# Kernel optimization log

Hardware: AMD Instinct MI355X
Metric: run time of the kernel (lower is better)

Reference implementation:

```python
import jax, jax.numpy as jnp
import numpy as np

B, N, H, D, F = 32, 128, 256, 256, 512   # batch, nodes, gru hidden, latent dim, mlp hidden
SUP = 0.5                                 # ancestor_suppression_strength
EPS = 1e-6


def _gru(x, h, Wx, Wh, bx, bh):
    """torch.nn.GRUCell math; x,h: [..., H]."""
    gx = x @ Wx + bx
    gh = h @ Wh + bh
    rx, ux, nx = jnp.split(gx, 3, axis=-1)
    rh, uh, nh = jnp.split(gh, 3, axis=-1)
    r = jax.nn.sigmoid(rx + rh)
    u = jax.nn.sigmoid(ux + uh)
    n = jnp.tanh(nx + r * nh)
    return (1.0 - u) * n + u * h


def setup_inputs() -> dict:
    key = jax.random.key(0)
    ks = jax.random.split(key, 12)
    rn = lambda k, shape, fan: jax.random.normal(k, shape, jnp.float32) * (fan ** -0.5)
    return {
        "z": jax.random.normal(ks[0], (B, D), jnp.float32),
        "targets": jax.random.randint(ks[1], (B, N, N), 0, 2, jnp.int32),
        "W_init": rn(ks[2], (D, H), D),
        "b_init": jnp.zeros((H,), jnp.float32),
        "Wx": rn(ks[3], (H, 3 * H), H),
        "Wh": rn(ks[4], (H, 3 * H), H),
        "bx": jnp.zeros((3 * H,), jnp.float32),
        "bh": jnp.zeros((3 * H,), jnp.float32),
        "W1": rn(ks[5], (2 * H + D, F), 2 * H + D),
        "b1": jnp.zeros((F,), jnp.float32),
        "W2": rn(ks[6], (F, 1), F),
        "b2": jnp.zeros((1,), jnp.float32),
    }


def reference(z, targets, W_init, b_init, Wx, Wh, bx, bh, W1, b1, W2, b2):
    # teacher-forcing link targets: strictly lower-triangular (parents have smaller index)
    tgt = jnp.tril(targets.astype(jnp.float32), k=-1)  # [B,N,N]
    idx = jnp.arange(N)

    def decode_one(z1, t1):  # z1:[D], t1:[N,N]
        h0 = jnp.tanh(z1 @ W_init + b_init)                      # decoder_init: z -> node-0 state
        states0 = jnp.zeros((N, H), jnp.float32).at[0].set(h0)
        A0 = jnp.zeros((N, N), jnp.float32)                      # ancestor bitset: A[i,j]=1 iff j ancestor of i

        def step(carry, t):
            states, A, ll = carry
            m = (idx < t).astype(jnp.float32)                    # existing-node mask
            pooled = (states * m[:, None]).sum(0) / m.sum()      # mean aggregation
            h_prov = _gru(pooled, h0, Wx, Wh, bx, bh)            # provisional new-node state
            # parent logits: MLP([h_new, h_j, z]) for every existing node j
            feat = jnp.concatenate([jnp.broadcast_to(h_prov, (N, H)), states,
                                    jnp.broadcast_to(z1, (N, D))], axis=-1)   # [N, 2H+D]
            logits = (jax.nn.relu(feat @ W1 + b1) @ W2 + b2)[:, 0]            # [N]
            row = t1[t]                                          # teacher-forced parents of node t
            anc = jnp.minimum(row @ A, 1.0)                      # j already ancestor of a chosen parent
            q = jnp.clip(jax.nn.sigmoid(logits) * (1.0 - SUP * anc), EPS, 1.0 - EPS)
            ll = ll + (m * (row * jnp.log(q) + (1.0 - row) * jnp.log1p(-q))).sum()
            A = A.at[t].set(jnp.minimum(row + row @ A, 1.0))     # ancestors(t) = parents U their ancestors
            states = states.at[t].set(h_prov)
            m2 = (idx <= t).astype(jnp.float32)[:, None]
            pooled2 = (states * m2).sum(0) / m2.sum()
            upd = _gru(jnp.broadcast_to(pooled2, (N, H)), states, Wx, Wh, bx, bh)
            states = m2 * upd + (1.0 - m2) * states              # propagate info among generated nodes
            return (states, A, ll), None

        (states, A, ll), _ = jax.lax.scan(step, (states0, A0, jnp.zeros((), jnp.float32)),
                                          jnp.arange(1, N))
        return t1, ll                                            # link matrix (teacher forced), log-likelihood

    L, ll = jax.vmap(decode_one)(z, tgt)
    return L, ll
```

## Files before the change

### kernel.cpp

```cpp
#include <hip/hip_runtime.h>
#include <hip/hip_bf16.h>
#include <math.h>

#define Bz 32
#define Nn 128
#define Hh 256
#define Dd 256
#define Ff 512
#define Gg 768
#define NT 512

typedef short v8s __attribute__((ext_vector_type(8)));
typedef float f4  __attribute__((ext_vector_type(4)));
#define MFMA(a,b,c) __builtin_amdgcn_mfma_f32_16x16x32_bf16(a,b,c,0,0,0)

#define WS_H0    0
#define WS_GH0   (WS_H0 + Bz*Hh)
#define WS_ZW1   (WS_GH0 + Bz*Gg)
#define WS_XH    (WS_ZW1 + Bz*Ff)
#define WS_PSX   (WS_XH + Bz*Hh)
#define WS_LOGP  (WS_PSX + Bz*Hh)
#define WS_BAR   (WS_LOGP + Bz*8*Nn)
#define WS_XS    (WS_BAR + Bz*32)
#define WS_WB    (WS_XS + Bz*16384)
#define WS_TOTAL (WS_WB + 160*2048)

#define SM_SW    0
#define SM_SST   81920
#define SM_NLDS  147456
#define SM_PS    155648
#define SM_HPF   156672
#define SM_GX1   157696
#define SM_GX2   158080
#define SM_BASE  158464
#define SM_BXS   158720
#define SM_BHS   159104
#define SM_GH0S  159488
#define SM_ZB1S  159872
#define SM_H0S   160128
#define SM_PSN   160256
#define SM_LOGI  160384
#define SM_ROWT  160896
#define SM_AMASK 161408
#define SM_ANCW  163456
#define SMEM_SZ  163488

__device__ __forceinline__ unsigned short f2bf(float x) {
  unsigned u = __float_as_uint(x);
  u = u + 0x7fffu + ((u >> 16) & 1u);
  return (unsigned short)(u >> 16);
}
__device__ __forceinline__ unsigned pack2(float e, float o) {
  return (unsigned)f2bf(e) | ((unsigned)f2bf(o) << 16);
}
__device__ __forceinline__ unsigned pkbf(float x, float y) {
  __hip_bfloat162 h = __float22bfloat162_rn(make_float2(x, y));
  union { __hip_bfloat162 h; unsigned u; } c; c.h = h; return c.u;
}
__device__ __forceinline__ float bf2f(unsigned short s) {
  return __uint_as_float(((unsigned)s) << 16);
}
__device__ __forceinline__ float sigm(float x) { return 1.0f / (1.0f + __expf(-x)); }
__device__ __forceinline__ float tanh_fast(float x) { return 2.0f / (1.0f + __expf(-2.0f*x)) - 1.0f; }
__device__ __forceinline__ v8s u4v(uint4 q) { union { uint4 q; v8s v; } c; c.q = q; return c.v; }

__device__ __forceinline__ void ast32(unsigned* p, unsigned v) {
  __hip_atomic_store(p, v, __ATOMIC_RELAXED, __HIP_MEMORY_SCOPE_AGENT);
}
__device__ __forceinline__ unsigned ald32(const unsigned* p) {
  return __hip_atomic_load(p, __ATOMIC_RELAXED, __HIP_MEMORY_SCOPE_AGENT);
}
__device__ __forceinline__ void ast64(unsigned long long* p, unsigned long long v) {
  __hip_atomic_store(p, v, __ATOMIC_RELAXED, __HIP_MEMORY_SCOPE_AGENT);
}
__device__ __forceinline__ unsigned long long ald64(const unsigned long long* p) {
  return __hip_atomic_load(p, __ATOMIC_RELAXED, __HIP_MEMORY_SCOPE_AGENT);
}

__device__ __forceinline__ void bbar(unsigned* cnt, unsigned& seq)
{
  __builtin_amdgcn_s_waitcnt(0x0F70);
  __syncthreads();
  seq += 8;
  if (threadIdx.x == 0) {
    __hip_atomic_fetch_add(cnt, 1u, __ATOMIC_RELAXED, __HIP_MEMORY_SCOPE_AGENT);
    while (__hip_atomic_load(cnt, __ATOMIC_RELAXED, __HIP_MEMORY_SCOPE_AGENT) < seq)
      __builtin_amdgcn_s_sleep(1);
  }
  __syncthreads();
}

__global__ void __launch_bounds__(256) prep_init(
    const int* __restrict__ tg, const float* __restrict__ Wx,
    const float* __restrict__ Wh, const float* __restrict__ W1,
    float* __restrict__ ws, float* __restrict__ out)
{
  const int stride = gridDim.x * blockDim.x;
  const int t0 = blockIdx.x * blockDim.x + threadIdx.x;

  for (int i = t0; i < Bz*Nn*Nn; i += stride) {
    int col = i & (Nn-1), row = (i >> 7) & (Nn-1);
    out[i] = (col < row) ? (float)tg[i] : 0.0f;
  }
  for (int i = t0; i < Bz; i += stride) out[Bz*Nn*Nn + i] = 0.0f;

  unsigned* BARu = (unsigned*)(ws + WS_BAR);
  for (int i = t0; i < Bz*32; i += stride) BARu[i] = 0u;

  unsigned* Wb = (unsigned*)(ws + WS_WB);
  for (int i = t0; i < 160*2048; i += stride) {
    int jw = i & 3, l = (i >> 2) & 63, ks = (i >> 8) & 7, nt = i >> 11;
    int k = ks*32 + (l >> 4)*8 + 2*jw;
    int n16 = l & 15;
    float lo, hi;
    if (nt < 48)       { int c = nt*16 + n16;        lo = Wh[k*Gg + c];      hi = Wh[(k+1)*Gg + c]; }
    else if (nt < 80)  { int f = (nt-48)*16 + n16;   lo = W1[(Hh+k)*Ff + f]; hi = W1[(Hh+k+1)*Ff + f]; }
    else if (nt < 128) { int c = (nt-80)*16 + n16;   lo = Wx[k*Gg + c];      hi = Wx[(k+1)*Gg + c]; }
    else               { int f = (nt-128)*16 + n16;  lo = W1[k*Ff + f];      hi = W1[(k+1)*Ff + f]; }
    Wb[i] = pack2(lo, hi);
  }
}

__global__ void __launch_bounds__(256) prep_batch(
    const float* __restrict__ z, const float* __restrict__ Wi,
    const float* __restrict__ bi, const float* __restrict__ Wh,
    const float* __restrict__ bh, const float* __restrict__ W1,
    float* __restrict__ ws)
{
  const int b = blockIdx.x, tid = threadIdx.x;
  __shared__ float zs[Dd], h0s[Hh];
  zs[tid] = z[b*Dd + tid];
  __syncthreads();
  float acc = bi[tid];
  for (int d = 0; d < Dd; ++d) acc = fmaf(zs[d], Wi[d*Hh + tid], acc);
  const float h0 = tanhf(acc);
  h0s[tid] = h0;
  ws[WS_H0 + b*Hh + tid] = h0;
  __syncthreads();
  for (int g = tid; g < Gg; g += 256) {
    float a = bh[g];
    for (int h = 0; h < Hh; ++h) a = fmaf(h0s[h], Wh[h*Gg + g], a);
    ws[WS_GH0 + b*Gg + g] = a;
  }
  for (int f = tid; f < Ff; f += 256) {
    float a = 0.0f;
    for (int d = 0; d < Dd; ++d) a = fmaf(zs[d], W1[(2*Hh + d)*Ff + f], a);
    ws[WS_ZW1 + b*Ff + f] = a;
  }
}

__device__ __forceinline__ void build_mv(const float* __restrict__ vec, int quad, v8s* av)
{
  #pragma unroll
  for (int ks = 0; ks < 8; ++ks) {
    const float4 a = *(const float4*)(vec + ks*32 + quad*8);
    const float4 c = *(const float4*)(vec + ks*32 + quad*8 + 4);
    union { unsigned u[4]; v8s v; } cv;
    cv.u[0] = pkbf(a.x, a.y); cv.u[1] = pkbf(a.z, a.w);
    cv.u[2] = pkbf(c.x, c.y); cv.u[3] = pkbf(c.z, c.w);
    av[ks] = cv.v;
  }
}
__device__ __forceinline__ void build_mv2(const float* __restrict__ va,
                                          const float* __restrict__ vb, int quad, v8s* av)
{
  #pragma unroll
  for (int ks = 0; ks < 8; ++ks) {
    const float4 a = *(const float4*)(va + ks*32 + quad*8);
    const float4 b = *(const float4*)(vb + ks*32 + quad*8);
    const float4 c = *(const float4*)(va + ks*32 + quad*8 + 4);
    const float4 d = *(const float4*)(vb + ks*32 + quad*8 + 4);
    union { unsigned u[4]; v8s v; } cv;
    cv.u[0] = pkbf(a.x+b.x, a.y+b.y); cv.u[1] = pkbf(a.z+b.z, a.w+b.w);
    cv.u[2] = pkbf(c.x+d.x, c.y+d.y); cv.u[3] = pkbf(c.z+d.z, c.w+d.w);
    av[ks] = cv.v;
  }
}

__global__ void __launch_bounds__(NT) decoder_main(
    const int* __restrict__ tg,
    const float* __restrict__ bx, const float* __restrict__ bh,
    const float* __restrict__ b1, const float* __restrict__ W2,
    const float* __restrict__ b2,
    float* __restrict__ ws, float* __restrict__ out)
{
  const int blk = blockIdx.x;
  const int b = blk & 31, r = blk >> 5;
  const int tid = threadIdx.x;
  const int lane = tid & 63, wv = tid >> 6;
  const int c16 = lane & 15, quad = lane >> 4;

  extern __shared__ char smem[];
  uint4* SW4 = (uint4*)(smem + SM_SW);
  unsigned short* SST = (unsigned short*)(smem + SM_SST);
  unsigned long long* SST64 = (unsigned long long*)(smem + SM_SST);
  unsigned short* NLDS = (unsigned short*)(smem + SM_NLDS);
  unsigned* NLDSu = (unsigned*)(smem + SM_NLDS);
  unsigned long long* NLDS64 = (unsigned long long*)(smem + SM_NLDS);
  float* PS   = (float*)(smem + SM_PS);
  float* HPF  = (float*)(smem + SM_HPF);
  float* GX1  = (float*)(smem + SM_GX1);
  float* GX2  = (float*)(smem + SM_GX2);
  float* BASE = (float*)(smem + SM_BASE);
  float* BXS  = (float*)(smem + SM_BXS);
  float* BHS  = (float*)(smem + SM_BHS);
  float* GH0S = (float*)(smem + SM_GH0S);
  float* ZB1S = (float*)(smem + SM_ZB1S);
  float* H0S  = (float*)(smem + SM_H0S);
  float* PSN  = (float*)(smem + SM_PSN);
  float* LOGI = (float*)(smem + SM_LOGI);
  float* ROWT = (float*)(smem + SM_ROWT);
  unsigned* AMASK = (unsigned*)(smem + SM_AMASK);
  unsigned* ANCW = (unsigned*)(smem + SM_ANCW);

  const float* __restrict__ h0g  = ws + WS_H0  + b*Hh;
  const float* __restrict__ gh0g = ws + WS_GH0 + b*Gg;
  const float* __restrict__ zW1g = ws + WS_ZW1 + b*Ff;
  unsigned* XHg  = (unsigned*)(ws + WS_XH) + b*Hh;
  unsigned long long* XH64 = (unsigned long long*)((unsigned*)(ws + WS_XH) + b*Hh);
  unsigned long long* PSX64 = (unsigned long long*)((unsigned*)(ws + WS_PSX) + b*Hh);
  unsigned long long* LOGP64 = (unsigned long long*)((unsigned*)(ws + WS_LOGP) + b*8*Nn);
  unsigned* LOGPg = (unsigned*)(ws + WS_LOGP) + b*8*Nn;
  unsigned* bar = (unsigned*)(ws + WS_BAR) + b*32;
  unsigned long long* XS64 = (unsigned long long*)(ws + WS_XS) + b*8192;
  const uint4* WB4 = (const uint4*)(ws + WS_WB);

  for (int i = tid; i < 16384; i += NT) ((unsigned*)SST)[i] = 0u;
  for (int i = tid; i < 5120; i += NT) {
    const int lt = i >> 9, q = i & 511;
    int gt;
    if (lt < 6) { const int gate = lt >> 1, tt = lt & 1; gt = gate*16 + 2*r + tt; }
    else        { gt = 48 + 4*r + (lt - 6); }
    SW4[lt*512 + q] = WB4[gt*512 + q];
  }
  if (tid < Hh) PS[tid] = h0g[tid];
  if (tid < 32) H0S[tid] = h0g[32*r + tid];
  if (tid < 96) {
    const int g = tid >> 5, hcl = tid & 31;
    const int col = g*256 + 32*r + hcl;
    BXS[tid] = bx[col]; BHS[tid] = bh[col]; GH0S[tid] = gh0g[col];
  }
  if (tid >= 96 && tid < 160) { const int f = 64*r + (tid - 96); ZB1S[tid-96] = zW1g[f] + b1[f]; }
  for (int i = tid; i < Nn*4; i += NT) AMASK[i] = 0u;
  float w2r[4];
  #pragma unroll
  for (int ft = 0; ft < 4; ++ft) w2r[ft] = W2[64*r + ft*16 + c16];
  const float b2v = b2[0];
  unsigned bseq = 0;
  __syncthreads();
  if (tid < Hh) {
    const int c = tid;
    SST[(c>>5)*512 + ((c>>3)&3)*128 + (c&7)] = f2bf(PS[c]);
  }
  __syncthreads();

  for (int t = 1; t < Nn; ++t) {
    const float invt  = 1.0f / (float)t;
    const float invt1 = 1.0f / (float)(t + 1);
    const int Mtot = (t + 16) >> 4;
    const int Mlog = (t + 15) >> 4;
    const int mtc = Mtot - 1;

    if (wv < 6) {
      v8s av[8]; build_mv(PS, quad, av);
      const int g = wv >> 1, tt = wv & 1;
      const uint4* Bp = WB4 + (80 + g*16 + 2*r + tt)*512 + lane;
      f4 c = {0.0f,0.0f,0.0f,0.0f};
      #pragma unroll
      for (int ks = 0; ks < 8; ++ks) c = MFMA(av[ks], u4v(Bp[ks*64]), c);
      if (quad == 0) GX1[g*32 + tt*16 + c16] = c[0];
    } else {
      const int j = tid - 384;
      ROWT[j] = (j < t) ? (float)tg[b*Nn*Nn + t*Nn + j] : 0.0f;
      LOGI[j] = 0.0f;
      if (j < 32) PSN[j] = 0.0f;
      if (j < 4) ANCW[j] = 0u;
    }
    __syncthreads();

    if (tid < 32) {
      const int hcl = tid;
      const float gxr = GX1[hcl]*invt    + BXS[hcl];
      const float gxu = GX1[32+hcl]*invt + BXS[32+hcl];
      const float gxn = GX1[64+hcl]*invt + BXS[64+hcl];
      const float rv = sigm(gxr + GH0S[hcl]);
      const float uv = sigm(gxu + GH0S[32+hcl]);
      const float nv = tanh_fast(gxn + rv*GH0S[64+hcl]);
      ast32(XHg + 32*r + hcl, __float_as_uint((1.0f-uv)*nv + uv*H0S[hcl]));
    }
    if (tid < Nn && tid < t && ROWT[tid] > 0.5f) {
      atomicOr(&ANCW[0], AMASK[tid*4+0]); atomicOr(&ANCW[1], AMASK[tid*4+1]);
      atomicOr(&ANCW[2], AMASK[tid*4+2]); atomicOr(&ANCW[3], AMASK[tid*4+3]);
    }
    bbar(bar, bseq);

    if (tid < 128) {
      const unsigned long long v = ald64(XH64 + tid);
      HPF[2*tid]   = __uint_as_float((unsigned)v);
      HPF[2*tid+1] = __uint_as_float((unsigned)(v >> 32));
    }
    __syncthreads();

    if (tid < 256) {
      const int c = tid;
      SST[(mtc*8 + (c>>5))*512 + (((c>>3)&3)*16 + (t&15))*8 + (c&7)] = f2bf(HPF[c]);
    } else {
      NLDSu[mtc*256 + (tid - 256)] = 0u;
    }
    if (wv < 2) {
      const unsigned long long bal = __ballot(tid < t && ROWT[tid] > 0.5f);
      if (lane == 0) {
        AMASK[t*4 + 2*wv]     = (unsigned)bal         | ANCW[2*wv];
        AMASK[t*4 + 2*wv + 1] = (unsigned)(bal >> 32) | ANCW[2*wv + 1];
      }
    }
    for (int j = wv; j < 10; j += 8) {
      if (j < 6) {
        v8s av[8]; build_mv2(PS, HPF, quad, av);
        const int g = j >> 1, tt = j & 1;
        const uint4* Bp = WB4 + (80 + g*16 + 2*r + tt)*512 + lane;
        f4 c = {0.0f,0.0f,0.0f,0.0f};
        #pragma unroll
        for (int ks = 0; ks < 8; ++ks) c = MFMA(av[ks], u4v(Bp[ks*64]), c);
        if (quad == 0) GX2[g*32 + tt*16 + c16] = c[0]*invt1 + BXS[g*32 + tt*16 + c16];
      } else {
        v8s av[8]; build_mv(HPF, quad, av);
        const int ft = j - 6;
        const uint4* Bp = WB4 + (128 + 4*r + ft)*512 + lane;
        f4 c = {0.0f,0.0f,0.0f,0.0f};
        #pragma unroll
        for (int ks = 0; ks < 8; ++ks) c = MFMA(av[ks], u4v(Bp[ks*64]), c);
        if (quad == 0) BASE[ft*16 + c16] = c[0] + ZB1S[ft*16 + c16];
      }
    }
    __syncthreads();

    const int nG = (Mtot + 1) >> 1;
    const int nL = (Mlog + 1) >> 1;
    const int njobs = nG + nL;
    for (int j = wv; j < njobs; j += 8) {
      if (j < nG) {
        const int mt0 = 2*j, mt1 = mt0 + 1;
        const bool do1 = (mt1 < Mtot);
        f4 acc[12];
        #pragma unroll
        for (int i = 0; i < 12; ++i) acc[i] = (f4){0.0f,0.0f,0.0f,0.0f};
        #pragma unroll
        for (int ks = 0; ks < 8; ++ks) {
          const v8s a0 = *(const v8s*)(SST + (mt0*8 + ks)*512 + lane*8);
          const v8s b0 = u4v(SW4[(0*8 + ks)*64 + lane]);
          const v8s b1 = u4v(SW4[(1*8 + ks)*64 + lane]);
          const v8s b2 = u4v(SW4[(2*8 + ks)*64 + lane]);
          const v8s b3 = u4v(SW4[(3*8 + ks)*64 + lane]);
          const v8s b4 = u4v(SW4[(4*8 + ks)*64 + lane]);
          const v8s b5 = u4v(SW4[(5*8 + ks)*64 + lane]);
          acc[0] = MFMA(a0, b0, acc[0]); acc[1] = MFMA(a0, b1, acc[1]);
          acc[2] = MFMA(a0, b2, acc[2]); acc[3] = MFMA(a0, b3, acc[3]);
          acc[4] = MFMA(a0, b4, acc[4]); acc[5] = MFMA(a0, b5, acc[5]);
          if (do1) {
            const v8s a1 = *(const v8s*)(SST + (mt1*8 + ks)*512 + lane*8);
            acc[6]  = MFMA(a1, b0, acc[6]);  acc[7]  = MFMA(a1, b1, acc[7]);
            acc[8]  = MFMA(a1, b2, acc[8]);  acc[9]  = MFMA(a1, b3, acc[9]);
            acc[10] = MFMA(a1, b4, acc[10]); acc[11] = MFMA(a1, b5, acc[11]);
          }
        }
        #pragma unroll
        for (int s = 0; s < 2; ++s) {
          if (s == 1 && !do1) break;
          const int mt = s ? mt1 : mt0;
          const f4* ac = acc + 6*s;
          #pragma unroll
          for (int ct = 0; ct < 2; ++ct) {
            const int hcl = ct*16 + c16;
            const f4 cr = ac[0 + ct], cu = ac[2 + ct], cn = ac[4 + ct];
            const float gxr = GX2[hcl], gxu = GX2[32+hcl], gxn = GX2[64+hcl];
            const float bhr = BHS[hcl], bhu = BHS[32+hcl], bhn = BHS[64+hcl];
            float colsum = 0.0f;
            #pragma unroll
            for (int rg = 0; rg < 4; ++rg) {
              const int row = mt*16 + quad*4 + rg;
              if (row <= t) {
                const int spi = ((hcl>>3)*16 + quad*4 + rg)*8 + (hcl & 7);
                const float old = bf2f(SST[(mt*8 + r)*512 + spi]);
                const float rv = sigm(gxr + cr[rg] + bhr);
                const float uv = sigm(gxu + cu[rg] + bhu);
                const float nv = tanh_fast(gxn + rv*(cn[rg] + bhn));
                const float ns = (1.0f-uv)*nv + uv*old;
                NLDS[mt*512 + spi] = f2bf(ns);
                colsum += ns;
              }
            }
            colsum += __shfl_down(colsum, 16);
            colsum += __shfl_down(colsum, 32);
            if (lane < 16) atomicAdd(&PSN[ct*16 + lane], colsum);
          }
        }
      } else {
        const int jj = j - nG;
        const int mt0 = 2*jj, mt1 = mt0 + 1;
        const bool do1 = (mt1 < Mlog);
        f4 acc[8];
        #pragma unroll
        for (int i = 0; i < 8; ++i) acc[i] = (f4){0.0f,0.0f,0.0f,0.0f};
        #pragma unroll
        for (int ks = 0; ks < 8; ++ks) {
          const v8s a0 = *(const v8s*)(SST + (mt0*8 + ks)*512 + lane*8);
          const v8s c0 = u4v(SW4[(6*8 + ks)*64 + lane]);
          const v8s c1 = u4v(SW4[(7*8 + ks)*64 + lane]);
          const v8s c2 = u4v(SW4[(8*8 + ks)*64 + lane]);
          const v8s c3 = u4v(SW4[(9*8 + ks)*64 + lane]);
          acc[0] = MFMA(a0, c0, acc[0]); acc[1] = MFMA(a0, c1, acc[1]);
          acc[2] = MFMA(a0, c2, acc[2]); acc[3] = MFMA(a0, c3, acc[3]);
          if (do1) {
            const v8s a1 = *(const v8s*)(SST + (mt1*8 + ks)*512 + lane*8);
            acc[4] = MFMA(a1, c0, acc[4]); acc[5] = MFMA(a1, c1, acc[5]);
            acc[6] = MFMA(a1, c2, acc[6]); acc[7] = MFMA(a1, c3, acc[7]);
          }
        }
        #pragma unroll
        for (int s = 0; s < 2; ++s) {
          if (s == 1 && !do1) break;
          const int mt = s ? mt1 : mt0;
          const f4* ac = acc + 4*s;
          #pragma unroll
          for (int rg = 0; rg < 4; ++rg) {
            float v = fmaxf(ac[0][rg] + BASE[c16],    0.0f)*w2r[0]
                    + fmaxf(ac[1][rg] + BASE[16+c16], 0.0f)*w2r[1]
                    + fmaxf(ac[2][rg] + BASE[32+c16], 0.0f)*w2r[2]
                    + fmaxf(ac[3][rg] + BASE[48+c16], 0.0f)*w2r[3];
            v += __shfl_xor(v, 1); v += __shfl_xor(v, 2);
            v += __shfl_xor(v, 4); v += __shfl_xor(v, 8);
            const int row = mt*16 + quad*4 + rg;
            if (c16 == 0 && row < t) atomicAdd(&LOGI[row], v);
          }
        }
      }
    }
    __syncthreads();

    for (int i = tid; i < Mtot*128; i += NT) {
      const int mt = i >> 7, q = i & 127;
      const unsigned long long v = NLDS64[i];
      ast64(XS64 + (mt*8 + r)*128 + q, v);
      SST64[(mt*8 + r)*128 + q] = v;
    }
    if (tid < 64) ast64(LOGP64 + r*64 + tid, ((const unsigned long long*)LOGI)[tid]);
    else if (tid < 80) ast64(PSX64 + r*16 + (tid - 64), ((const unsigned long long*)PSN)[tid - 64]);
    bbar(bar, bseq);

    for (int i = tid; i < Mtot*1024; i += NT) {
      const int ks = (i >> 7) & 7;
      if (ks != r) SST64[i] = ald64(XS64 + i);
    }
    if (tid < 128) {
      const unsigned long long v = ald64(PSX64 + tid);
      PS[2*tid]   = __uint_as_float((unsigned)v);
      PS[2*tid+1] = __uint_as_float((unsigned)(v >> 32));
    }
    if (r == (t & 7)) {
      float term = 0.0f;
      if (tid < t) {
        float lsum = b2v;
        #pragma unroll
        for (int rr = 0; rr < 8; ++rr)
          lsum += __uint_as_float(ald32(LOGPg + rr*Nn + tid));
        const float anc = (float)((ANCW[tid >> 5] >> (tid & 31)) & 1u);
        float q = sigm(lsum) * (1.0f - 0.5f*anc);
        q = fminf(fmaxf(q, 1e-6f), 1.0f - 1e-6f);
        term = ROWT[tid]*logf(q) + (1.0f - ROWT[tid])*log1pf(-q);
      }
      if (wv < 2) {
        #pragma unroll
        for (int off = 32; off; off >>= 1) term += __shfl_down(term, off);
        if (lane == 0) atomicAdd(&out[Bz*Nn*Nn + b], term);
      }
    }
    __syncthreads();
  }
}

extern "C" void kernel_launch(void* const* d_in, const int* in_sizes, int n_in,
                              void* d_out, int out_size, void* d_ws, size_t ws_size,
                              hipStream_t stream)
{
  const float* z  = (const float*)d_in[0];
  const int*   tg = (const int*)  d_in[1];
  const float* Wi = (const float*)d_in[2];
  const float* bi = (const float*)d_in[3];
  const float* Wx = (const float*)d_in[4];
  const float* Wh = (const float*)d_in[5];
  const float* bx = (const float*)d_in[6];
  const float* bh = (const float*)d_in[7];
  const float* W1 = (const float*)d_in[8];
  const float* b1 = (const float*)d_in[9];
  const float* W2 = (const float*)d_in[10];
  const float* b2 = (const float*)d_in[11];
  float* out = (float*)d_out;
  float* ws  = (float*)d_ws;

  hipFuncSetAttribute((const void*)decoder_main,
                      hipFuncAttributeMaxDynamicSharedMemorySize, SMEM_SZ);

  hipLaunchKernelGGL(prep_init, dim3(512), dim3(256), 0, stream, tg, Wx, Wh, W1, ws, out);
  hipLaunchKernelGGL(prep_batch, dim3(Bz), dim3(256), 0, stream, z, Wi, bi, Wh, bh, W1, ws);

  void* args[] = { (void*)&tg, (void*)&bx, (void*)&bh, (void*)&b1,
                   (void*)&W2, (void*)&b2, (void*)&ws, (void*)&out };
  hipLaunchCooperativeKernel((void*)decoder_main, dim3(256), dim3(NT),
                             args, SMEM_SZ, stream);
}
```

Baseline: 1.970 ms.

## Merge per-step grid barriers by exchanging partial gate projections instead of states

```diff
diff --git a/kernel.cpp b/kernel.cpp
--- a/kernel.cpp
+++ b/kernel.cpp
@@ -17,33 +17,26 @@
 #define WS_H0    0
 #define WS_GH0   (WS_H0 + Bz*Hh)
 #define WS_ZW1   (WS_GH0 + Bz*Gg)
-#define WS_XH    (WS_ZW1 + Bz*Ff)
-#define WS_PSX   (WS_XH + Bz*Hh)
-#define WS_LOGP  (WS_PSX + Bz*Hh)
+#define WS_GXP   (WS_ZW1 + Bz*Ff)
+#define WS_LOGP  (WS_GXP + Bz*8*Gg)
 #define WS_BAR   (WS_LOGP + Bz*8*Nn)
 #define WS_XS    (WS_BAR + Bz*32)
 #define WS_WB    (WS_XS + Bz*16384)
-#define WS_TOTAL (WS_WB + 160*2048)
 
 #define SM_SW    0
 #define SM_SST   81920
 #define SM_NLDS  147456
-#define SM_PS    155648
-#define SM_HPF   156672
-#define SM_GX1   157696
-#define SM_GX2   158080
-#define SM_BASE  158464
-#define SM_BXS   158720
-#define SM_BHS   159104
-#define SM_GH0S  159488
-#define SM_ZB1S  159872
-#define SM_H0S   160128
+#define SM_GXF   155648
+#define SM_HPF   158720
+#define SM_GX2   159232
+#define SM_BASE  159616
+#define SM_BHS   159872
 #define SM_PSN   160256
 #define SM_LOGI  160384
-#define SM_ROWT  160896
-#define SM_AMASK 161408
-#define SM_ANCW  163456
-#define SMEM_SZ  163488
+#define SM_RBIT  160896
+#define SM_ANCW  160928
+#define SM_AMASK 160960
+#define SMEM_SZ  163008
 
 __device__ __forceinline__ unsigned short f2bf(float x) {
   unsigned u = __float_as_uint(x);
@@ -149,34 +142,6 @@
   }
 }
 
-__device__ __forceinline__ void build_mv(const float* __restrict__ vec, int quad, v8s* av)
-{
-  #pragma unroll
-  for (int ks = 0; ks < 8; ++ks) {
-    const float4 a = *(const float4*)(vec + ks*32 + quad*8);
-    const float4 c = *(const float4*)(vec + ks*32 + quad*8 + 4);
-    union { unsigned u[4]; v8s v; } cv;
-    cv.u[0] = pkbf(a.x, a.y); cv.u[1] = pkbf(a.z, a.w);
-    cv.u[2] = pkbf(c.x, c.y); cv.u[3] = pkbf(c.z, c.w);
-    av[ks] = cv.v;
-  }
-}
-__device__ __forceinline__ void build_mv2(const float* __restrict__ va,
-                                          const float* __restrict__ vb, int quad, v8s* av)
-{
-  #pragma unroll
-  for (int ks = 0; ks < 8; ++ks) {
-    const float4 a = *(const float4*)(va + ks*32 + quad*8);
-    const float4 b = *(const float4*)(vb + ks*32 + quad*8);
-    const float4 c = *(const float4*)(va + ks*32 + quad*8 + 4);
-    const float4 d = *(const float4*)(vb + ks*32 + quad*8 + 4);
-    union { unsigned u[4]; v8s v; } cv;
-    cv.u[0] = pkbf(a.x+b.x, a.y+b.y); cv.u[1] = pkbf(a.z+b.z, a.w+b.w);
-    cv.u[2] = pkbf(c.x+d.x, c.y+d.y); cv.u[3] = pkbf(c.z+d.z, c.w+d.w);
-    av[ks] = cv.v;
-  }
-}
-
 __global__ void __launch_bounds__(NT) decoder_main(
     const int* __restrict__ tg,
     const float* __restrict__ bx, const float* __restrict__ bh,
@@ -197,30 +162,24 @@
   unsigned short* NLDS = (unsigned short*)(smem + SM_NLDS);
   unsigned* NLDSu = (unsigned*)(smem + SM_NLDS);
   unsigned long long* NLDS64 = (unsigned long long*)(smem + SM_NLDS);
-  float* PS   = (float*)(smem + SM_PS);
-  float* HPF  = (float*)(smem + SM_HPF);
-  float* GX1  = (float*)(smem + SM_GX1);
+  float* GXF  = (float*)(smem + SM_GXF);
+  unsigned short* HPF = (unsigned short*)(smem + SM_HPF);
   float* GX2  = (float*)(smem + SM_GX2);
   float* BASE = (float*)(smem + SM_BASE);
-  float* BXS  = (float*)(smem + SM_BXS);
   float* BHS  = (float*)(smem + SM_BHS);
-  float* GH0S = (float*)(smem + SM_GH0S);
-  float* ZB1S = (float*)(smem + SM_ZB1S);
-  float* H0S  = (float*)(smem + SM_H0S);
   float* PSN  = (float*)(smem + SM_PSN);
   float* LOGI = (float*)(smem + SM_LOGI);
-  float* ROWT = (float*)(smem + SM_ROWT);
+  unsigned* RBIT  = (unsigned*)(smem + SM_RBIT);
+  unsigned* ANCW  = (unsigned*)(smem + SM_ANCW);
   unsigned* AMASK = (unsigned*)(smem + SM_AMASK);
-  unsigned* ANCW = (unsigned*)(smem + SM_ANCW);
 
   const float* __restrict__ h0g  = ws + WS_H0  + b*Hh;
   const float* __restrict__ gh0g = ws + WS_GH0 + b*Gg;
   const float* __restrict__ zW1g = ws + WS_ZW1 + b*Ff;
-  unsigned* XHg  = (unsigned*)(ws + WS_XH) + b*Hh;
-  unsigned long long* XH64 = (unsigned long long*)((unsigned*)(ws + WS_XH) + b*Hh);
-  unsigned long long* PSX64 = (unsigned long long*)((unsigned*)(ws + WS_PSX) + b*Hh);
-  unsigned long long* LOGP64 = (unsigned long long*)((unsigned*)(ws + WS_LOGP) + b*8*Nn);
+  unsigned* GXPown = (unsigned*)(ws + WS_GXP) + b*8*Gg + r*Gg;
+  const unsigned long long* GXP64 = (const unsigned long long*)((unsigned*)(ws + WS_GXP) + b*8*Gg);
   unsigned* LOGPg = (unsigned*)(ws + WS_LOGP) + b*8*Nn;
+  unsigned long long* LOGP64 = (unsigned long long*)LOGPg;
   unsigned* bar = (unsigned*)(ws + WS_BAR) + b*32;
   unsigned long long* XS64 = (unsigned long long*)(ws + WS_XS) + b*8192;
   const uint4* WB4 = (const uint4*)(ws + WS_WB);
@@ -233,15 +192,8 @@
     else        { gt = 48 + 4*r + (lt - 6); }
     SW4[lt*512 + q] = WB4[gt*512 + q];
   }
-  if (tid < Hh) PS[tid] = h0g[tid];
-  if (tid < 32) H0S[tid] = h0g[32*r + tid];
-  if (tid < 96) {
-    const int g = tid >> 5, hcl = tid & 31;
-    const int col = g*256 + 32*r + hcl;
-    BXS[tid] = bx[col]; BHS[tid] = bh[col]; GH0S[tid] = gh0g[col];
-  }
-  if (tid >= 96 && tid < 160) { const int f = 64*r + (tid - 96); ZB1S[tid-96] = zW1g[f] + b1[f]; }
   for (int i = tid; i < Nn*4; i += NT) AMASK[i] = 0u;
+  if (tid < 96) BHS[tid] = bh[(tid >> 5)*256 + 32*r + (tid & 31)];
   float w2r[4];
   #pragma unroll
   for (int ft = 0; ft < 4; ++ft) w2r[ft] = W2[64*r + ft*16 + c16];
@@ -250,87 +202,138 @@
   __syncthreads();
   if (tid < Hh) {
     const int c = tid;
-    SST[(c>>5)*512 + ((c>>3)&3)*128 + (c&7)] = f2bf(PS[c]);
-  }
+    SST[(c>>5)*512 + ((c>>3)&3)*128 + (c&7)] = f2bf(h0g[c]);
+  }
+  if (tid < 32) PSN[tid] = h0g[32*r + tid];
   __syncthreads();
+  {
+    union { unsigned u[4]; v8s v; } cv;
+    const float4 a0 = *(const float4*)(PSN + quad*8);
+    const float4 a1 = *(const float4*)(PSN + quad*8 + 4);
+    cv.u[0] = pkbf(a0.x, a0.y); cv.u[1] = pkbf(a0.z, a0.w);
+    cv.u[2] = pkbf(a1.x, a1.y); cv.u[3] = pkbf(a1.z, a1.w);
+    const v8s avp = cv.v;
+    #pragma unroll
+    for (int k2 = 0; k2 < 6; ++k2) {
+      const int nt = wv*6 + k2;
+      f4 c = {0.0f,0.0f,0.0f,0.0f};
+      c = MFMA(avp, u4v(WB4[(80 + nt)*512 + r*64 + lane]), c);
+      if (quad == 0) ast32(GXPown + nt*16 + c16, __float_as_uint(c[0]));
+    }
+  }
+  if (tid < 128) ast64(XS64 + r*128 + tid, SST64[r*128 + tid]);
+  bbar(bar, bseq);
 
   for (int t = 1; t < Nn; ++t) {
+    const int par = (t & 1) * 4;
     const float invt  = 1.0f / (float)t;
     const float invt1 = 1.0f / (float)(t + 1);
     const int Mtot = (t + 16) >> 4;
     const int Mlog = (t + 15) >> 4;
     const int mtc = Mtot - 1;
 
-    if (wv < 6) {
-      v8s av[8]; build_mv(PS, quad, av);
-      const int g = wv >> 1, tt = wv & 1;
-      const uint4* Bp = WB4 + (80 + g*16 + 2*r + tt)*512 + lane;
-      f4 c = {0.0f,0.0f,0.0f,0.0f};
+    for (int i = tid; i < Mlog*1024; i += NT) {
+      if (((i >> 7) & 7) != r) SST64[i] = ald64(XS64 + i);
+    }
+    if (tid < 384) {
+      float s0 = 0.0f, s1 = 0.0f;
       #pragma unroll
-      for (int ks = 0; ks < 8; ++ks) c = MFMA(av[ks], u4v(Bp[ks*64]), c);
-      if (quad == 0) GX1[g*32 + tt*16 + c16] = c[0];
+      for (int rr = 0; rr < 8; ++rr) {
+        const unsigned long long v = ald64(GXP64 + rr*384 + tid);
+        s0 += __uint_as_float((unsigned)v);
+        s1 += __uint_as_float((unsigned)(v >> 32));
+      }
+      GXF[2*tid]   = s0;
+      GXF[2*tid+1] = s1;
     } else {
       const int j = tid - 384;
-      ROWT[j] = (j < t) ? (float)tg[b*Nn*Nn + t*Nn + j] : 0.0f;
+      const int val = (j < t) ? tg[b*Nn*Nn + t*Nn + j] : 0;
+      const unsigned long long bal = __ballot(val != 0);
+      if (lane == 0) {
+        RBIT[par + (wv - 6)*2]     = (unsigned)bal;
+        RBIT[par + (wv - 6)*2 + 1] = (unsigned)(bal >> 32);
+      }
       LOGI[j] = 0.0f;
       if (j < 32) PSN[j] = 0.0f;
-      if (j < 4) ANCW[j] = 0u;
+      if (j < 4) ANCW[par + j] = 0u;
+    }
+    if (t > 1 && r == ((t - 1) & 7)) {
+      const int pp = par ^ 4;
+      float term = 0.0f;
+      if (tid < (t - 1)) {
+        float lsum = b2v;
+        #pragma unroll
+        for (int rr = 0; rr < 8; ++rr)
+          lsum += __uint_as_float(ald32(LOGPg + rr*Nn + tid));
+        const float anc = (float)((ANCW[pp + (tid >> 5)] >> (tid & 31)) & 1u);
+        float q = sigm(lsum) * (1.0f - 0.5f*anc);
+        q = fminf(fmaxf(q, 1e-6f), 1.0f - 1e-6f);
+        const unsigned rb = (RBIT[pp + (tid >> 5)] >> (tid & 31)) & 1u;
+        term = rb ? logf(q) : log1pf(-q);
+      }
+      if (wv < 2) {
+        #pragma unroll
+        for (int off = 32; off; off >>= 1) term += __shfl_down(term, off);
+        if (lane == 0) atomicAdd(&out[Bz*Nn*Nn + b], term);
+      }
     }
     __syncthreads();
 
-    if (tid < 32) {
-      const int hcl = tid;
-      const float gxr = GX1[hcl]*invt    + BXS[hcl];
-      const float gxu = GX1[32+hcl]*invt + BXS[32+hcl];
-      const float gxn = GX1[64+hcl]*invt + BXS[64+hcl];
-      const float rv = sigm(gxr + GH0S[hcl]);
-      const float uv = sigm(gxu + GH0S[32+hcl]);
-      const float nv = tanh_fast(gxn + rv*GH0S[64+hcl]);
-      ast32(XHg + 32*r + hcl, __float_as_uint((1.0f-uv)*nv + uv*H0S[hcl]));
-    }
-    if (tid < Nn && tid < t && ROWT[tid] > 0.5f) {
-      atomicOr(&ANCW[0], AMASK[tid*4+0]); atomicOr(&ANCW[1], AMASK[tid*4+1]);
-      atomicOr(&ANCW[2], AMASK[tid*4+2]); atomicOr(&ANCW[3], AMASK[tid*4+3]);
-    }
-    bbar(bar, bseq);
-
-    if (tid < 128) {
-      const unsigned long long v = ald64(XH64 + tid);
-      HPF[2*tid]   = __uint_as_float((unsigned)v);
-      HPF[2*tid+1] = __uint_as_float((unsigned)(v >> 32));
+    if (tid < 256) {
+      const int hc = tid;
+      const float rv = sigm(GXF[hc]*invt + bx[hc] + gh0g[hc]);
+      const float uv = sigm(GXF[256+hc]*invt + bx[256+hc] + gh0g[256+hc]);
+      const float nv = tanh_fast(GXF[512+hc]*invt + bx[512+hc] + rv*gh0g[512+hc]);
+      HPF[hc] = f2bf((1.0f - uv)*nv + uv*h0g[hc]);
+    } else if (tid < 384) {
+      const int j = tid - 256;
+      if (j < t && ((RBIT[par + (j >> 5)] >> (j & 31)) & 1u)) {
+        atomicOr(&ANCW[par+0], AMASK[j*4+0]); atomicOr(&ANCW[par+1], AMASK[j*4+1]);
+        atomicOr(&ANCW[par+2], AMASK[j*4+2]); atomicOr(&ANCW[par+3], AMASK[j*4+3]);
+      }
     }
     __syncthreads();
 
     if (tid < 256) {
       const int c = tid;
-      SST[(mtc*8 + (c>>5))*512 + (((c>>3)&3)*16 + (t&15))*8 + (c&7)] = f2bf(HPF[c]);
+      SST[(mtc*8 + (c>>5))*512 + (((c>>3)&3)*16 + (t&15))*8 + (c&7)] = HPF[c];
     } else {
       NLDSu[mtc*256 + (tid - 256)] = 0u;
     }
     if (wv < 2) {
-      const unsigned long long bal = __ballot(tid < t && ROWT[tid] > 0.5f);
+      const unsigned rbv = (RBIT[par + (tid >> 5)] >> (tid & 31)) & 1u;
+      const unsigned long long bal = __ballot(tid < t && rbv);
       if (lane == 0) {
-        AMASK[t*4 + 2*wv]     = (unsigned)bal         | ANCW[2*wv];
-        AMASK[t*4 + 2*wv + 1] = (unsigned)(bal >> 32) | ANCW[2*wv + 1];
-      }
-    }
-    for (int j = wv; j < 10; j += 8) {
-      if (j < 6) {
-        v8s av[8]; build_mv2(PS, HPF, quad, av);
-        const int g = j >> 1, tt = j & 1;
-        const uint4* Bp = WB4 + (80 + g*16 + 2*r + tt)*512 + lane;
-        f4 c = {0.0f,0.0f,0.0f,0.0f};
-        #pragma unroll
-        for (int ks = 0; ks < 8; ++ks) c = MFMA(av[ks], u4v(Bp[ks*64]), c);
-        if (quad == 0) GX2[g*32 + tt*16 + c16] = c[0]*invt1 + BXS[g*32 + tt*16 + c16];
-      } else {
-        v8s av[8]; build_mv(HPF, quad, av);
-        const int ft = j - 6;
-        const uint4* Bp = WB4 + (128 + 4*r + ft)*512 + lane;
-        f4 c = {0.0f,0.0f,0.0f,0.0f};
-        #pragma unroll
-        for (int ks = 0; ks < 8; ++ks) c = MFMA(av[ks], u4v(Bp[ks*64]), c);
-        if (quad == 0) BASE[ft*16 + c16] = c[0] + ZB1S[ft*16 + c16];
+        AMASK[t*4 + 2*wv]     = (unsigned)bal         | ANCW[par + 2*wv];
+        AMASK[t*4 + 2*wv + 1] = (unsigned)(bal >> 32) | ANCW[par + 2*wv + 1];
+      }
+    }
+    {
+      v8s av[8];
+      #pragma unroll
+      for (int ks = 0; ks < 8; ++ks) av[ks] = *(const v8s*)(HPF + ks*32 + quad*8);
+      for (int j = wv; j < 10; j += 8) {
+        if (j < 6) {
+          const int g = j >> 1, tt = j & 1;
+          const uint4* Bp = WB4 + (80 + g*16 + 2*r + tt)*512 + lane;
+          f4 c = {0.0f,0.0f,0.0f,0.0f};
+          #pragma unroll
+          for (int ks = 0; ks < 8; ++ks) c = MFMA(av[ks], u4v(Bp[ks*64]), c);
+          if (quad == 0) {
+            const int col = g*256 + 32*r + tt*16 + c16;
+            GX2[g*32 + tt*16 + c16] = (c[0] + GXF[col])*invt1 + bx[col];
+          }
+        } else {
+          const int ft = j - 6;
+          const uint4* Bp = WB4 + (128 + 4*r + ft)*512 + lane;
+          f4 c = {0.0f,0.0f,0.0f,0.0f};
+          #pragma unroll
+          for (int ks = 0; ks < 8; ++ks) c = MFMA(av[ks], u4v(Bp[ks*64]), c);
+          if (quad == 0) {
+            const int f = 64*r + ft*16 + c16;
+            BASE[ft*16 + c16] = c[0] + zW1g[f] + b1[f];
+          }
+        }
       }
     }
     __syncthreads();
@@ -349,18 +352,18 @@
         for (int ks = 0; ks < 8; ++ks) {
           const v8s a0 = *(const v8s*)(SST + (mt0*8 + ks)*512 + lane*8);
           const v8s b0 = u4v(SW4[(0*8 + ks)*64 + lane]);
-          const v8s b1 = u4v(SW4[(1*8 + ks)*64 + lane]);
-          const v8s b2 = u4v(SW4[(2*8 + ks)*64 + lane]);
+          const v8s b1v = u4v(SW4[(1*8 + ks)*64 + lane]);
+          const v8s b2v2 = u4v(SW4[(2*8 + ks)*64 + lane]);
           const v8s b3 = u4v(SW4[(3*8 + ks)*64 + lane]);
           const v8s b4 = u4v(SW4[(4*8 + ks)*64 + lane]);
           const v8s b5 = u4v(SW4[(5*8 + ks)*64 + lane]);
-          acc[0] = MFMA(a0, b0, acc[0]); acc[1] = MFMA(a0, b1, acc[1]);
-          acc[2] = MFMA(a0, b2, acc[2]); acc[3] = MFMA(a0, b3, acc[3]);
+          acc[0] = MFMA(a0, b0, acc[0]); acc[1] = MFMA(a0, b1v, acc[1]);
+          acc[2] = MFMA(a0, b2v2, acc[2]); acc[3] = MFMA(a0, b3, acc[3]);
           acc[4] = MFMA(a0, b4, acc[4]); acc[5] = MFMA(a0, b5, acc[5]);
           if (do1) {
             const v8s a1 = *(const v8s*)(SST + (mt1*8 + ks)*512 + lane*8);
-            acc[6]  = MFMA(a1, b0, acc[6]);  acc[7]  = MFMA(a1, b1, acc[7]);
-            acc[8]  = MFMA(a1, b2, acc[8]);  acc[9]  = MFMA(a1, b3, acc[9]);
+            acc[6]  = MFMA(a1, b0, acc[6]);  acc[7]  = MFMA(a1, b1v, acc[7]);
+            acc[8]  = MFMA(a1, b2v2, acc[8]);  acc[9]  = MFMA(a1, b3, acc[9]);
             acc[10] = MFMA(a1, b4, acc[10]); acc[11] = MFMA(a1, b5, acc[11]);
           }
         }
@@ -438,6 +441,21 @@
     }
     __syncthreads();
 
+    {
+      union { unsigned u[4]; v8s v; } cv;
+      const float4 a0 = *(const float4*)(PSN + quad*8);
+      const float4 a1 = *(const float4*)(PSN + quad*8 + 4);
+      cv.u[0] = pkbf(a0.x, a0.y); cv.u[1] = pkbf(a0.z, a0.w);
+      cv.u[2] = pkbf(a1.x, a1.y); cv.u[3] = pkbf(a1.z, a1.w);
+      const v8s avp = cv.v;
+      #pragma unroll
+      for (int k2 = 0; k2 < 6; ++k2) {
+        const int nt = wv*6 + k2;
+        f4 c = {0.0f,0.0f,0.0f,0.0f};
+        c = MFMA(avp, u4v(WB4[(80 + nt)*512 + r*64 + lane]), c);
+        if (quad == 0) ast32(GXPown + nt*16 + c16, __float_as_uint(c[0]));
+      }
+    }
     for (int i = tid; i < Mtot*128; i += NT) {
       const int mt = i >> 7, q = i & 127;
       const unsigned long long v = NLDS64[i];
@@ -445,37 +463,29 @@
       SST64[(mt*8 + r)*128 + q] = v;
     }
     if (tid < 64) ast64(LOGP64 + r*64 + tid, ((const unsigned long long*)LOGI)[tid]);
-    else if (tid < 80) ast64(PSX64 + r*16 + (tid - 64), ((const unsigned long long*)PSN)[tid - 64]);
     bbar(bar, bseq);
-
-    for (int i = tid; i < Mtot*1024; i += NT) {
-      const int ks = (i >> 7) & 7;
-      if (ks != r) SST64[i] = ald64(XS64 + i);
-    }
-    if (tid < 128) {
-      const unsigned long long v = ald64(PSX64 + tid);
-      PS[2*tid]   = __uint_as_float((unsigned)v);
-      PS[2*tid+1] = __uint_as_float((unsigned)(v >> 32));
-    }
-    if (r == (t & 7)) {
-      float term = 0.0f;
-      if (tid < t) {
-        float lsum = b2v;
-        #pragma unroll
-        for (int rr = 0; rr < 8; ++rr)
-          lsum += __uint_as_float(ald32(LOGPg + rr*Nn + tid));
-        const float anc = (float)((ANCW[tid >> 5] >> (tid & 31)) & 1u);
-        float q = sigm(lsum) * (1.0f - 0.5f*anc);
-        q = fminf(fmaxf(q, 1e-6f), 1.0f - 1e-6f);
-        term = ROWT[tid]*logf(q) + (1.0f - ROWT[tid])*log1pf(-q);
-      }
-      if (wv < 2) {
-        #pragma unroll
-        for (int off = 32; off; off >>= 1) term += __shfl_down(term, off);
-        if (lane == 0) atomicAdd(&out[Bz*Nn*Nn + b], term);
-      }
-    }
-    __syncthreads();
+  }
+
+  if (r == 7) {
+    const int tl = Nn - 1;
+    const int pp = (tl & 1) * 4;
+    float term = 0.0f;
+    if (tid < tl) {
+      float lsum = b2v;
+      #pragma unroll
+      for (int rr = 0; rr < 8; ++rr)
+        lsum += __uint_as_float(ald32(LOGPg + rr*Nn + tid));
+      const float anc = (float)((ANCW[pp + (tid >> 5)] >> (tid & 31)) & 1u);
+      float q = sigm(lsum) * (1.0f - 0.5f*anc);
+      q = fminf(fmaxf(q, 1e-6f), 1.0f - 1e-6f);
+      const unsigned rb = (RBIT[pp + (tid >> 5)] >> (tid & 31)) & 1u;
+      term = rb ? logf(q) : log1pf(-q);
+    }
+    if (wv < 2) {
+      #pragma unroll
+      for (int off = 32; off; off >>= 1) term += __shfl_down(term, off);
+      if (lane == 0) atomicAdd(&out[Bz*Nn*Nn + b], term);
+    }
   }
 }
 
```

Measured after the change: 2.044 ms. +3.7%, slower.
